# Kernel optimization log

Hardware: AMD Instinct MI355X
Metric: run time of the kernel (lower is better)

The kernel has to match this reference:

```python
import jax, jax.numpy as jnp
import numpy as np

KS = 3          # kernel_size
NH = 6          # num_heads
NUM_TOK = KS ** 3  # 27 neighbors per query


def setup_inputs() -> dict:
    key = jax.random.key(0)
    k1, k2, k3 = jax.random.split(key, 3)
    q = jax.random.normal(k1, (1, 40, 40, 40, 96), dtype=jnp.float32)
    k = jax.random.normal(k2, (1, 40, 40, 40, 96), dtype=jnp.float32)
    rpb = jax.random.normal(k3, (NH, KS, KS, KS), dtype=jnp.float32) * 0.02
    return {"q": q, "k": k, "rpb": rpb}


def _offsets():
    # torch.arange(-3//2+1, 3//2+1) == arange(-1, 2); meshgrid 'ij'; stacked -> [27, 3]
    r = jnp.arange(-1, 2, dtype=jnp.float32)
    g = jnp.stack(jnp.meshgrid(r, r, r, indexing="ij"), axis=-1)
    return g.reshape(NUM_TOK, 3)


def reference(q, k, rpb):
    B, H, W, T, C = q.shape
    hd = C // NH
    scale = hd ** -0.5
    N = H * W * T

    # queries: [B, N, nh, hd], pre-scaled
    qh = q.reshape(B, N, NH, hd) * scale

    # zero-pad keys by 1 voxel on each spatial side (matches nnf.pad on channels-first k)
    kp = jnp.pad(jnp.transpose(k, (0, 4, 1, 2, 3)),
                 ((0, 0), (0, 0), (1, 1), (1, 1), (1, 1)))

    # 27 shifted views == torch unfold over a 3x3x3 window (i slowest, matches grid order)
    wins = [kp[:, :, i:i + H, j:j + W, l:l + T]
            for i in range(KS) for j in range(KS) for l in range(KS)]
    Kw = jnp.stack(wins, axis=2)                 # [B, C, 27, H, W, T]
    Kw = Kw.reshape(B, NH, hd, NUM_TOK, N)        # [B, nh, hd, 27, N]

    # attention logits over the 27-token neighborhood
    attn = jnp.einsum("bnhd,bhdkn->bnhk", qh, Kw)  # [B, N, nh, 27]
    attn = attn + rpb.reshape(NH, NUM_TOK)[None, None, :, :]  # relative position bias
    attn = jax.nn.softmax(attn, axis=-1)

    # expected displacement: weighted sum of integer offsets -> [B, N, nh, 3]
    x = jnp.einsum("bnhk,kc->bnhc", attn, _offsets())
    x = x.reshape(B, H, W, T, NH * 3)
    return jnp.transpose(x, (0, 4, 1, 2, 3))      # [B, nh*3, H, W, T]
```

## Files before the change

### kernel.cpp

```cpp
#include <hip/hip_runtime.h>

typedef _Float16 hh2 __attribute__((ext_vector_type(2)));

#define DH 40
#define DW 40
#define DT 40
#define NC 96
#define NH 6
#define HD 16
#define NTOK 27
#define NVOX (DH * DW * DT)

#define TX 8
#define TY 8
#define TZ 8
#define HX 10
#define HY 10
#define HZ 10
#define NHALO 1000

#define TXN 5
#define TYN 5
#define TZN 5
#define NTILE 125
#define NJOB 750
#define GRID 752
#define PER_XCD 94

__device__ __forceinline__ float dot2acc(hh2 a, hh2 b, float c) {
    return __builtin_amdgcn_fdot2(a, b, c, false);
}
__device__ __forceinline__ hh2 pkrtz(float a, float b) {
    return __builtin_bit_cast(hh2, __builtin_amdgcn_cvt_pkrtz(a, b));
}
__device__ __forceinline__ unsigned int pkbits(float a, float b) {
    return __builtin_bit_cast(unsigned int, __builtin_amdgcn_cvt_pkrtz(a, b));
}

union I4H {
    int4 v[2];
    hh2 h[8];
};

__global__ __launch_bounds__(512, 4) void natt_disp_kernel(
    const float* __restrict__ q,
    const float* __restrict__ k,
    const float* __restrict__ rpb,
    float* __restrict__ out)
{
    __shared__ int4 s_k[NHALO * 2];

    const int job = (blockIdx.x & 7) * PER_XCD + (blockIdx.x >> 3);
    if (job >= NJOB) return;

    const int h    = job % NH;
    const int tile = job / NH;
    const int tz = tile % TZN;
    const int ty = (tile / TZN) % TYN;
    const int tx = tile / (TZN * TYN);
    const int x0 = tx * TX, y0 = ty * TY, z0 = tz * TZ;

    const int tid = threadIdx.x;

    float rk[NTOK];
    {
        const float* rb = rpb + h * NTOK;
        #pragma unroll
        for (int kk = 0; kk < NTOK; ++kk) rk[kk] = rb[kk];
    }

    const float* kh = k + h * HD;

    #pragma unroll
    for (int it = 0; it < 8; ++it) {
        const int jj = tid + it * 512;
        if (jj < NHALO * 4) {
            const int n = jj >> 2;
            const int c = jj & 3;
            const int hx = n / (HY * HZ);
            const int r  = n - hx * (HY * HZ);
            const int hy = r / HZ;
            const int hz = r - hy * HZ;
            const int gx = x0 - 1 + hx;
            const int gy = y0 - 1 + hy;
            const int gz = z0 - 1 + hz;
            uint2 w; w.x = 0u; w.y = 0u;
            if (((unsigned)gx < DH) & ((unsigned)gy < DW) & ((unsigned)gz < DT)) {
                const float4 a = *(const float4*)(
                    kh + ((size_t)((gx * DW + gy) * DT + gz)) * NC + c * 4);
                w.x = pkbits(a.x, a.y);
                w.y = pkbits(a.z, a.w);
            }
            const int p = hy & 1;
            ((uint2*)s_k)[((n * 2 + (c >> 1)) ^ p) * 2 + (c & 1)] = w;
        }
    }

    const int lz = tid & 7;
    const int ly = (tid >> 3) & 7;
    const int lx = tid >> 6;
    const int vox = ((x0 + lx) * DW + (y0 + ly)) * DT + (z0 + lz);

    hh2 qh[8];
    {
        const float4* qv = (const float4*)(q + (size_t)vox * NC + h * HD);
        const float4 a = qv[0], b = qv[1], c = qv[2], d = qv[3];
        qh[0] = pkrtz(a.x, a.y);
        qh[1] = pkrtz(a.z, a.w);
        qh[2] = pkrtz(b.x, b.y);
        qh[3] = pkrtz(b.z, b.w);
        qh[4] = pkrtz(c.x, c.y);
        qh[5] = pkrtz(c.z, c.w);
        qh[6] = pkrtz(d.x, d.y);
        qh[7] = pkrtz(d.z, d.w);
    }

    __syncthreads();

    const float SC2 = 0.36067376f;
    const float LOG2E = 1.44269504f;
    float sum = 0.f, sx = 0.f, sy = 0.f, sz = 0.f;

    #pragma unroll
    for (int i = 0; i < 3; ++i) {
        #pragma unroll
        for (int j = 0; j < 3; ++j) {
            const int base = ((lx + i) * HY + (ly + j)) * HZ + lz;
            const int p = (ly + j) & 1;
            #pragma unroll
            for (int ll = 0; ll < 3; ++ll) {
                const int n = base + ll;
                I4H u;
                u.v[0] = s_k[(n * 2 + 0) ^ p];
                u.v[1] = s_k[(n * 2 + 1) ^ p];
                float d = 0.0f;
                d = dot2acc(qh[0], u.h[0], d);
                d = dot2acc(qh[1], u.h[1], d);
                d = dot2acc(qh[2], u.h[2], d);
                d = dot2acc(qh[3], u.h[3], d);
                d = dot2acc(qh[4], u.h[4], d);
                d = dot2acc(qh[5], u.h[5], d);
                d = dot2acc(qh[6], u.h[6], d);
                d = dot2acc(qh[7], u.h[7], d);
                const int kk = (i * 3 + j) * 3 + ll;
                const float t = exp2f(fmaf(d, SC2, rk[kk] * LOG2E));
                sum += t;
                if (i == 0) sx -= t; else if (i == 2) sx += t;
                if (j == 0) sy -= t; else if (j == 2) sy += t;
                if (ll == 0) sz -= t; else if (ll == 2) sz += t;
            }
        }
    }

    const float inv = __builtin_amdgcn_rcpf(sum);

    out[((size_t)(h * 3 + 0)) * NVOX + vox] = sx * inv;
    out[((size_t)(h * 3 + 1)) * NVOX + vox] = sy * inv;
    out[((size_t)(h * 3 + 2)) * NVOX + vox] = sz * inv;
}

extern "C" void kernel_launch(void* const* d_in, const int* in_sizes, int n_in,
                              void* d_out, int out_size, void* d_ws, size_t ws_size,
                              hipStream_t stream) {
    const float* q   = (const float*)d_in[0];
    const float* k   = (const float*)d_in[1];
    const float* rpb = (const float*)d_in[2];
    float* out = (float*)d_out;

    natt_disp_kernel<<<GRID, 512, 0, stream>>>(q, k, rpb, out);
}
```

Baseline: 20.28 us.

## Compute two z-adjacent voxels per thread to share key LDS reads

Each thread now handles two neighbouring voxels along z, so each key row is read once from LDS and used for both queries (4 reads per row instead of 6). The block shrinks to 256 threads, the halo load loop doubles its trip count, and the LDS swizzle changes to a wider XOR pattern. The bias is pre-scaled by log2e when loaded. The aim is to cut LDS traffic and per-voxel overhead, at the cost of more registers per thread and fewer threads available to hide the halo load latency.

```diff
diff --git a/kernel.cpp b/kernel.cpp
--- a/kernel.cpp
+++ b/kernel.cpp
@@ -22,7 +22,6 @@
 #define TXN 5
 #define TYN 5
 #define TZN 5
-#define NTILE 125
 #define NJOB 750
 #define GRID 752
 #define PER_XCD 94
@@ -35,6 +34,10 @@
 }
 __device__ __forceinline__ unsigned int pkbits(float a, float b) {
     return __builtin_bit_cast(unsigned int, __builtin_amdgcn_cvt_pkrtz(a, b));
+}
+
+__device__ __forceinline__ int phys(int n, int m) {
+    return (2 * n + m) ^ ((n >> 1) & 7);
 }
 
 union I4H {
@@ -42,7 +45,7 @@
     hh2 h[8];
 };
 
-__global__ __launch_bounds__(512, 4) void natt_disp_kernel(
+__global__ __launch_bounds__(256, 4) void natt_disp_kernel(
     const float* __restrict__ q,
     const float* __restrict__ k,
     const float* __restrict__ rpb,
@@ -62,18 +65,19 @@
 
     const int tid = threadIdx.x;
 
+    const float LOG2E = 1.44269504f;
     float rk[NTOK];
     {
         const float* rb = rpb + h * NTOK;
         #pragma unroll
-        for (int kk = 0; kk < NTOK; ++kk) rk[kk] = rb[kk];
+        for (int kk = 0; kk < NTOK; ++kk) rk[kk] = rb[kk] * LOG2E;
     }
 
     const float* kh = k + h * HD;
 
     #pragma unroll
-    for (int it = 0; it < 8; ++it) {
-        const int jj = tid + it * 512;
+    for (int it = 0; it < 16; ++it) {
+        const int jj = tid + it * 256;
         if (jj < NHALO * 4) {
             const int n = jj >> 2;
             const int c = jj & 3;
@@ -91,72 +95,97 @@
                 w.x = pkbits(a.x, a.y);
                 w.y = pkbits(a.z, a.w);
             }
-            const int p = hy & 1;
-            ((uint2*)s_k)[((n * 2 + (c >> 1)) ^ p) * 2 + (c & 1)] = w;
+            ((uint2*)s_k)[phys(n, c >> 1) * 2 + (c & 1)] = w;
         }
     }
 
-    const int lz = tid & 7;
-    const int ly = (tid >> 3) & 7;
-    const int lx = tid >> 6;
-    const int vox = ((x0 + lx) * DW + (y0 + ly)) * DT + (z0 + lz);
-
-    hh2 qh[8];
+    const int za = tid & 3;
+    const int ly = (tid >> 2) & 7;
+    const int lx = tid >> 5;
+    const int vox0 = ((x0 + lx) * DW + (y0 + ly)) * DT + (z0 + 2 * za);
+    const int vox1 = vox0 + 1;
+
+    hh2 qh0[8], qh1[8];
     {
-        const float4* qv = (const float4*)(q + (size_t)vox * NC + h * HD);
+        const float4* qv = (const float4*)(q + (size_t)vox0 * NC + h * HD);
         const float4 a = qv[0], b = qv[1], c = qv[2], d = qv[3];
-        qh[0] = pkrtz(a.x, a.y);
-        qh[1] = pkrtz(a.z, a.w);
-        qh[2] = pkrtz(b.x, b.y);
-        qh[3] = pkrtz(b.z, b.w);
-        qh[4] = pkrtz(c.x, c.y);
-        qh[5] = pkrtz(c.z, c.w);
-        qh[6] = pkrtz(d.x, d.y);
-        qh[7] = pkrtz(d.z, d.w);
+        qh0[0] = pkrtz(a.x, a.y); qh0[1] = pkrtz(a.z, a.w);
+        qh0[2] = pkrtz(b.x, b.y); qh0[3] = pkrtz(b.z, b.w);
+        qh0[4] = pkrtz(c.x, c.y); qh0[5] = pkrtz(c.z, c.w);
+        qh0[6] = pkrtz(d.x, d.y); qh0[7] = pkrtz(d.z, d.w);
+    }
+    {
+        const float4* qv = (const float4*)(q + (size_t)vox1 * NC + h * HD);
+        const float4 a = qv[0], b = qv[1], c = qv[2], d = qv[3];
+        qh1[0] = pkrtz(a.x, a.y); qh1[1] = pkrtz(a.z, a.w);
+        qh1[2] = pkrtz(b.x, b.y); qh1[3] = pkrtz(b.z, b.w);
+        qh1[4] = pkrtz(c.x, c.y); qh1[5] = pkrtz(c.z, c.w);
+        qh1[6] = pkrtz(d.x, d.y); qh1[7] = pkrtz(d.z, d.w);
     }
 
     __syncthreads();
 
     const float SC2 = 0.36067376f;
-    const float LOG2E = 1.44269504f;
-    float sum = 0.f, sx = 0.f, sy = 0.f, sz = 0.f;
+    float s0 = 0.f, sx0 = 0.f, sy0 = 0.f, sz0 = 0.f;
+    float s1 = 0.f, sx1 = 0.f, sy1 = 0.f, sz1 = 0.f;
 
     #pragma unroll
     for (int i = 0; i < 3; ++i) {
         #pragma unroll
         for (int j = 0; j < 3; ++j) {
-            const int base = ((lx + i) * HY + (ly + j)) * HZ + lz;
-            const int p = (ly + j) & 1;
+            const int base = ((lx + i) * HY + (ly + j)) * HZ + 2 * za;
+            const int kb = (i * 3 + j) * 3;
             #pragma unroll
-            for (int ll = 0; ll < 3; ++ll) {
-                const int n = base + ll;
+            for (int r = 0; r < 4; ++r) {
+                const int n = base + r;
                 I4H u;
-                u.v[0] = s_k[(n * 2 + 0) ^ p];
-                u.v[1] = s_k[(n * 2 + 1) ^ p];
-                float d = 0.0f;
-                d = dot2acc(qh[0], u.h[0], d);
-                d = dot2acc(qh[1], u.h[1], d);
-                d = dot2acc(qh[2], u.h[2], d);
-                d = dot2acc(qh[3], u.h[3], d);
-                d = dot2acc(qh[4], u.h[4], d);
-                d = dot2acc(qh[5], u.h[5], d);
-                d = dot2acc(qh[6], u.h[6], d);
-                d = dot2acc(qh[7], u.h[7], d);
-                const int kk = (i * 3 + j) * 3 + ll;
-                const float t = exp2f(fmaf(d, SC2, rk[kk] * LOG2E));
-                sum += t;
-                if (i == 0) sx -= t; else if (i == 2) sx += t;
-                if (j == 0) sy -= t; else if (j == 2) sy += t;
-                if (ll == 0) sz -= t; else if (ll == 2) sz += t;
+                u.v[0] = s_k[phys(n, 0)];
+                u.v[1] = s_k[phys(n, 1)];
+                if (r <= 2) {
+                    float d = 0.0f;
+                    d = dot2acc(qh0[0], u.h[0], d);
+                    d = dot2acc(qh0[1], u.h[1], d);
+                    d = dot2acc(qh0[2], u.h[2], d);
+                    d = dot2acc(qh0[3], u.h[3], d);
+                    d = dot2acc(qh0[4], u.h[4], d);
+                    d = dot2acc(qh0[5], u.h[5], d);
+                    d = dot2acc(qh0[6], u.h[6], d);
+                    d = dot2acc(qh0[7], u.h[7], d);
+                    const float t = exp2f(fmaf(d, SC2, rk[kb + r]));
+                    s0 += t;
+                    if (i == 0) sx0 -= t; else if (i == 2) sx0 += t;
+                    if (j == 0) sy0 -= t; else if (j == 2) sy0 += t;
+                    if (r == 0) sz0 -= t; else if (r == 2) sz0 += t;
+                }
+                if (r >= 1) {
+                    float d = 0.0f;
+                    d = dot2acc(qh1[0], u.h[0], d);
+                    d = dot2acc(qh1[1], u.h[1], d);
+                    d = dot2acc(qh1[2], u.h[2], d);
+                    d = dot2acc(qh1[3], u.h[3], d);
+                    d = dot2acc(qh1[4], u.h[4], d);
+                    d = dot2acc(qh1[5], u.h[5], d);
+                    d = dot2acc(qh1[6], u.h[6], d);
+                    d = dot2acc(qh1[7], u.h[7], d);
+                    const float t = exp2f(fmaf(d, SC2, rk[kb + r - 1]));
+                    s1 += t;
+                    if (i == 0) sx1 -= t; else if (i == 2) sx1 += t;
+                    if (j == 0) sy1 -= t; else if (j == 2) sy1 += t;
+                    if (r == 1) sz1 -= t; else if (r == 3) sz1 += t;
+                }
             }
         }
     }
 
-    const float inv = __builtin_amdgcn_rcpf(sum);
-
-    out[((size_t)(h * 3 + 0)) * NVOX + vox] = sx * inv;
-    out[((size_t)(h * 3 + 1)) * NVOX + vox] = sy * inv;
-    out[((size_t)(h * 3 + 2)) * NVOX + vox] = sz * inv;
+    const float i0 = __builtin_amdgcn_rcpf(s0);
+    const float i1 = __builtin_amdgcn_rcpf(s1);
+
+    out[((size_t)(h * 3 + 0)) * NVOX + vox0] = sx0 * i0;
+    out[((size_t)(h * 3 + 1)) * NVOX + vox0] = sy0 * i0;
+    out[((size_t)(h * 3 + 2)) * NVOX + vox0] = sz0 * i0;
+    out[((size_t)(h * 3 + 0)) * NVOX + vox1] = sx1 * i1;
+    out[((size_t)(h * 3 + 1)) * NVOX + vox1] = sy1 * i1;
+    out[((size_t)(h * 3 + 2)) * NVOX + vox1] = sz1 * i1;
 }
 
 extern "C" void kernel_launch(void* const* d_in, const int* in_sizes, int n_in,
@@ -167,5 +196,5 @@
     const float* rpb = (const float*)d_in[2];
     float* out = (float*)d_out;
 
-    natt_disp_kernel<<<GRID, 512, 0, stream>>>(q, k, rpb, out);
-}
+    natt_disp_kernel<<<GRID, 256, 0, stream>>>(q, k, rpb, out);
+}
```

After: 24.09 us. 18.8% more time.
